# Kernel tuning notes

Measured on AMD Instinct MI355X. Metric: run time of the kernel, lower is better.

Reference implementation:

```python
import jax, jax.numpy as jnp
import numpy as np

Bsz, T, N, Dm = 4, 256, 32, 128
L, S, DC = 2, 16, 4          # num_layers, d_state, d_conv
DI = 2 * Dm                   # d_inner (expand=2)
DTR = Dm // 16                # dt_rank = ceil(128/16) = 8
K, R = 4, 16                  # K_bases, rank
MAX_DT = 0.2

def _silu(x):
    return x * jax.nn.sigmoid(x)

def _causal_dwconv(x, w, b):
    # x: [BN, T, DI], w: [DI, DC] depthwise, left-pad DC-1 (== pad DC-1 both sides then [:T])
    xc = jnp.swapaxes(x, 1, 2)  # [BN, DI, T]
    y = jax.lax.conv_general_dilated(xc, w[:, None, :], (1,), [(DC - 1, 0)],
                                     feature_group_count=DI,
                                     dimension_numbers=('NCH', 'OIH', 'NCH'))
    return jnp.swapaxes(y + b[None, :, None], 1, 2)

def _selective_scan(x, dt, Bm, Cm, A):
    # x, dt: [BN,T,DI]; Bm, Cm: [BN,T,S]; A: [DI,S]
    def step(carry, inp):
        dt_t, B_t, C_t, x_t = inp
        dA = jnp.exp(dt_t[:, :, None] * A)                      # [BN,DI,S]
        carry = dA * carry + dt_t[:, :, None] * B_t[:, None, :] * x_t[:, :, None]
        y = jnp.einsum('bds,bs->bd', carry, C_t)
        return carry, y
    BN = x.shape[0]
    carry0 = jnp.zeros((BN, DI, S), x.dtype)
    seq = (jnp.swapaxes(dt, 0, 1), jnp.swapaxes(Bm, 0, 1),
           jnp.swapaxes(Cm, 0, 1), jnp.swapaxes(x, 0, 1))
    _, ys = jax.lax.scan(step, carry0, seq)
    return jnp.swapaxes(ys, 0, 1)

def _mamba(h, in_w, cw, cb, xw, dtw, dtb, A_log, Dp, ow):
    xz = h @ in_w.T                          # [BN,T,2*DI]
    xh, z = xz[..., :DI], xz[..., DI:]
    xh = _silu(_causal_dwconv(xh, cw, cb))
    x_dbl = xh @ xw.T                        # [BN,T,DTR+2S]
    dt = jax.nn.softplus(x_dbl[..., :DTR] @ dtw.T + dtb)
    Bm = x_dbl[..., DTR:DTR + S]
    Cm = x_dbl[..., DTR + S:]
    A = -jnp.exp(A_log)
    y = _selective_scan(xh, dt, Bm, Cm, A) + Dp * xh
    return (y * _silu(z)) @ ow.T

def setup_inputs():
    ks = jax.random.split(jax.random.key(0), 32)
    n = lambda i, shp, s: jax.random.normal(ks[i], shp, jnp.float32) * s
    sD = 1.0 / np.sqrt(Dm); sI = 1.0 / np.sqrt(DI)
    return {
        'x': n(0, (Bsz, T, N, Dm), 1.0),
        'in_proj_w': n(1, (L, 2 * DI, Dm), sD),
        'conv_w': n(2, (L, DI, DC), 1.0 / np.sqrt(DC)),
        'conv_b': n(3, (L, DI), 0.01),
        'x_proj_w': n(4, (L, DTR + 2 * S, DI), sI),
        'dt_proj_w': n(5, (L, DI, DTR), 1.0 / np.sqrt(DTR)),
        'dt_proj_b': jnp.full((L, DI), -4.0, jnp.float32) + n(6, (L, DI), 0.1),
        'A_log': jnp.tile(jnp.log(jnp.arange(1, S + 1, dtype=jnp.float32))[None, None, :], (L, DI, 1)),
        'D_skip': jnp.ones((L, DI), jnp.float32),
        'out_proj_w': n(7, (L, Dm, DI), sI),
        'U': n(8, (K, Dm, R), sD),
        'V': n(9, (K, R, Dm), sD),
        'A_scale': jnp.full((K,), 0.3, jnp.float32),
        'gate_w1': n(10, (Dm, Dm), sD), 'gate_b1': jnp.zeros((Dm,), jnp.float32),
        'gate_w2': n(11, (K + 1, Dm), sD), 'gate_b2': jnp.zeros((K + 1,), jnp.float32),
        'film_g_w': n(12, (Dm, Dm), sD), 'film_g_b': jnp.zeros((Dm,), jnp.float32),
        'film_b_w': n(13, (Dm, Dm), sD), 'film_b_b': jnp.zeros((Dm,), jnp.float32),
        'mix_w1': n(14, (Dm, Dm), sD), 'mix_b1': jnp.zeros((Dm,), jnp.float32),
        'mix_w2': n(15, (1, Dm), sD), 'mix_b2': jnp.zeros((1,), jnp.float32),
    }

def reference(x, in_proj_w, conv_w, conv_b, x_proj_w, dt_proj_w, dt_proj_b, A_log, D_skip, out_proj_w, U, V, A_scale, gate_w1, gate_b1, gate_w2, gate_b2, film_g_w, film_g_b, film_b_w, film_b_b, mix_w1, mix_b1, mix_w2, mix_b2):
    B, T_, N_, D_ = x.shape
    h = x.transpose(0, 2, 1, 3).reshape(B * N_, T_, D_)   # [BN,T,D]
    for l in range(L):  # residual Mamba stack
        h = h + _mamba(h, in_proj_w[l], conv_w[l], conv_b[l], x_proj_w[l],
                       dt_proj_w[l], dt_proj_b[l], A_log[l], D_skip[l], out_proj_w[l])
    gate_out = jax.nn.gelu(h @ gate_w1.T + gate_b1, approximate=False) @ gate_w2.T + gate_b2
    w = jax.nn.softmax(gate_out[..., :K], axis=-1)        # [BN,T,K]
    dt = jax.nn.sigmoid(gate_out[..., K:]) * MAX_DT       # [BN,T,1]
    U_eff = U * A_scale[:, None, None]
    def amix(hh):
        hU = jnp.einsum('btd,kdr->btkr', hh, U_eff)
        hUV = jnp.einsum('btkr,krd->btkd', hU, V)
        return jnp.einsum('btkd,btk->btd', hUV, w)
    hA = amix(h)
    hA2 = amix(hA)  # taylor_order == 2
    upd_nl = jnp.tanh(dt * hA + 0.5 * dt ** 2 * hA2)
    gamma = jnp.tanh(h @ film_g_w.T + film_g_b)
    beta = jnp.tanh(h @ film_b_w.T + film_b_b)
    upd_nl = gamma * upd_nl + beta
    g = jax.nn.sigmoid(jax.nn.gelu(h @ mix_w1.T + mix_b1, approximate=False) @ mix_w2.T + mix_b2)
    h_dyn = h + g * upd_nl
    return h_dyn.reshape(B, N_, T_, D_).transpose(0, 2, 1, 3)
```

## Files before the change

kernel.cpp:

```cpp
#include <hip/hip_runtime.h>
#include <math.h>

#define BSZ   4
#define TT    256
#define NN    32
#define DM    128
#define LL    2
#define SS    16
#define DCV   4
#define DI    256
#define DTR   8
#define KK    4
#define RR    16
#define BN_   128
#define TOK   32768

typedef _Float16 f16x8 __attribute__((ext_vector_type(8)));
typedef float    f32x4 __attribute__((ext_vector_type(4)));

__device__ __forceinline__ float sigm(float x) { return __fdividef(1.f, 1.f + __expf(-x)); }

__global__ __launch_bounds__(256) void pack_h_k(const float* __restrict__ x, float* __restrict__ h)
{
    int tid = threadIdx.x;
    int d = tid & 127;
    int tok = blockIdx.x * 2 + (tid >> 7);
    int t = tok & 255;
    int bn = tok >> 8;
    int b = bn >> 5, n = bn & 31;
    h[(size_t)tok * DM + d] = x[(((size_t)b * TT + t) * NN + n) * DM + d];
}

template<int EPI, int ACT>
__global__ __launch_bounds__(256)
void mgemm_k(const float* __restrict__ A, int lda,
             const float* __restrict__ W,
             const float* __restrict__ bias,
             float* C, int ldc,
             int N, int K,
             const float* __restrict__ aux, int auxb)
{
    __shared__ char smem[24576];

    const int tid  = threadIdx.x;
    const int lane = tid & 63;
    const int wv   = tid >> 6;
    const long row0 = (long)blockIdx.y * 128;
    const int  colb = blockIdx.x * 64;
    const int  NC   = K >> 5;

    const int st_rc = tid >> 2;
    const int st_g  = tid & 3;
    const int offA0 = st_rc * 64        + ((st_g ^ (st_rc & 3)) << 4);
    const int offA1 = (st_rc + 64) * 64 + ((st_g ^ (st_rc & 3)) << 4);
    const int offW  = st_rc * 64        + ((st_g ^ (st_rc & 3)) << 4);
    const int wcol  = colb + st_rc;
    const bool wok  = (wcol < N);

    const int fr = lane & 15;
    const int fg = lane >> 4;
    const int ra0 = (wv << 5) + fr;
    const int offa0 = ra0 * 64        + ((fg ^ (ra0 & 3)) << 4);
    const int offa1 = (ra0 + 16) * 64 + ((fg ^ (ra0 & 3)) << 4);
    int offb[4];
#pragma unroll
    for (int nj = 0; nj < 4; ++nj) {
        int cb = (nj << 4) + fr;
        offb[nj] = cb * 64 + ((fg ^ (fr & 3)) << 4);
    }

    f32x4 acc[2][4];
#pragma unroll
    for (int mi = 0; mi < 2; ++mi)
#pragma unroll
        for (int nj = 0; nj < 4; ++nj) acc[mi][nj] = (f32x4){0.f, 0.f, 0.f, 0.f};

    float va0[8], va1[8], vw[8];

    {
        const float* pa0 = A + (row0 + st_rc) * (long)lda + st_g * 8;
        *(float4*)&va0[0] = *(const float4*)pa0;
        *(float4*)&va0[4] = *(const float4*)(pa0 + 4);
        const float* pa1 = pa0 + 64 * (long)lda;
        *(float4*)&va1[0] = *(const float4*)pa1;
        *(float4*)&va1[4] = *(const float4*)(pa1 + 4);
        if (wok) {
            const float* pw = W + (long)wcol * K + st_g * 8;
            *(float4*)&vw[0] = *(const float4*)pw;
            *(float4*)&vw[4] = *(const float4*)(pw + 4);
        } else {
#pragma unroll
            for (int j = 0; j < 8; ++j) vw[j] = 0.f;
        }
    }
    {
        char* base = smem;
        f16x8 h0, h1, hw;
#pragma unroll
        for (int j = 0; j < 8; ++j) { h0[j] = (_Float16)va0[j]; h1[j] = (_Float16)va1[j]; hw[j] = (_Float16)vw[j]; }
        *(f16x8*)(base + offA0) = h0;
        *(f16x8*)(base + offA1) = h1;
        *(f16x8*)(base + 8192 + offW) = hw;
    }
    __syncthreads();

    for (int c = 0; c < NC; ++c) {
        if (c + 1 < NC) {
            const int kk = (c + 1) << 5;
            const float* pa0 = A + (row0 + st_rc) * (long)lda + kk + st_g * 8;
            *(float4*)&va0[0] = *(const float4*)pa0;
            *(float4*)&va0[4] = *(const float4*)(pa0 + 4);
            const float* pa1 = pa0 + 64 * (long)lda;
            *(float4*)&va1[0] = *(const float4*)pa1;
            *(float4*)&va1[4] = *(const float4*)(pa1 + 4);
            if (wok) {
                const float* pw = W + (long)wcol * K + kk + st_g * 8;
                *(float4*)&vw[0] = *(const float4*)pw;
                *(float4*)&vw[4] = *(const float4*)(pw + 4);
            }
        }
        {
            const char* As = smem + (c & 1) * 12288;
            const char* Ws = As + 8192;
            f16x8 af0 = *(const f16x8*)(As + offa0);
            f16x8 af1 = *(const f16x8*)(As + offa1);
            f16x8 bf[4];
#pragma unroll
            for (int nj = 0; nj < 4; ++nj) bf[nj] = *(const f16x8*)(Ws + offb[nj]);
#pragma unroll
            for (int nj = 0; nj < 4; ++nj) {
                acc[0][nj] = __builtin_amdgcn_mfma_f32_16x16x32_f16(af0, bf[nj], acc[0][nj], 0, 0, 0);
                acc[1][nj] = __builtin_amdgcn_mfma_f32_16x16x32_f16(af1, bf[nj], acc[1][nj], 0, 0, 0);
            }
        }
        if (c + 1 < NC) {
            char* base = smem + ((c + 1) & 1) * 12288;
            f16x8 h0, h1, hw;
#pragma unroll
            for (int j = 0; j < 8; ++j) { h0[j] = (_Float16)va0[j]; h1[j] = (_Float16)va1[j]; hw[j] = (_Float16)vw[j]; }
            *(f16x8*)(base + offA0) = h0;
            *(f16x8*)(base + offA1) = h1;
            *(f16x8*)(base + 8192 + offW) = hw;
        }
        __syncthreads();
    }

#pragma unroll
    for (int nj = 0; nj < 4; ++nj) {
        int col = colb + (nj << 4) + fr;
        if (col < N) {
            float bb = 0.f;
            if (EPI == 1 && bias) bb = bias[col];
#pragma unroll
            for (int mi = 0; mi < 2; ++mi) {
                long rg = row0 + (wv << 5) + (mi << 4) + (fg << 2);
#pragma unroll
                for (int r = 0; r < 4; ++r) {
                    float v = acc[mi][nj][r];
                    if (EPI == 1) {
                        v += bb;
                        if (ACT == 1) v = 0.5f * v * (1.f + erff(v * 0.70710678118654752f));
                        else if (ACT == 2) v = tanhf(v);
                    } else if (EPI == 6) {
                        v *= aux[(rg + r) * 4 + ((col >> 4) + auxb)];
                    }
                    float* pc = C + (rg + r) * (long)ldc + col;
                    if (EPI == 4) *pc += v;
                    else          *pc = v;
                }
            }
        }
    }
}

template<int BM, int BN, int TM, int TN, int EPI>
__global__ __launch_bounds__(256)
void gemm_k(const float* __restrict__ A, int lda,
            const float* __restrict__ W,
            const float* __restrict__ bias,
            float* C, int ldc,
            int M, int N, int K,
            const float* __restrict__ aux)
{
    constexpr int BK = 16;
    constexpr int LDS_A = BM + 4;
    constexpr int LDS_B = BN + 4;
    static_assert((BM / TM) * (BN / TN) == 256, "256 threads");
    constexpr int NA = BM * BK / 1024;
    constexpr int NB = BN * BK / 1024;

    __shared__ float As[BK][LDS_A];
    __shared__ float Ws[BK][LDS_B];

    const int tid = threadIdx.x;
    constexpr int nx = BN / TN;
    const int tx = tid % nx, ty = tid / nx;
    const long row0 = (long)blockIdx.y * BM;
    const long col0 = (long)blockIdx.x * BN;

    float acc[TM][TN];
#pragma unroll
    for (int i = 0; i < TM; i++)
#pragma unroll
        for (int j = 0; j < TN; j++) acc[i][j] = 0.f;

    for (int kk = 0; kk < K; kk += BK) {
        float4 a_reg[NA], w_reg[NB];
#pragma unroll
        for (int i = 0; i < NA; ++i) {
            int idx = i * 1024 + tid * 4;
            int r = idx >> 4, k0 = idx & 15;
            int k = kk + k0;
            const float* p = A + (row0 + r) * (long)lda + k;
            a_reg[i] = *(const float4*)p;
        }
#pragma unroll
        for (int i = 0; i < NB; ++i) {
            int idx = i * 1024 + tid * 4;
            int r = idx >> 4, k0 = idx & 15;
            long gc = col0 + r;
            int k = kk + k0;
            if (gc < N) {
                const float* p = W + gc * (long)K + k;
                w_reg[i] = *(const float4*)p;
            } else w_reg[i] = make_float4(0.f, 0.f, 0.f, 0.f);
        }
        __syncthreads();
#pragma unroll
        for (int i = 0; i < NA; ++i) {
            int idx = i * 1024 + tid * 4;
            int r = idx >> 4, k0 = idx & 15;
            As[k0 + 0][r] = a_reg[i].x; As[k0 + 1][r] = a_reg[i].y;
            As[k0 + 2][r] = a_reg[i].z; As[k0 + 3][r] = a_reg[i].w;
        }
#pragma unroll
        for (int i = 0; i < NB; ++i) {
            int idx = i * 1024 + tid * 4;
            int r = idx >> 4, k0 = idx & 15;
            Ws[k0 + 0][r] = w_reg[i].x; Ws[k0 + 1][r] = w_reg[i].y;
            Ws[k0 + 2][r] = w_reg[i].z; Ws[k0 + 3][r] = w_reg[i].w;
        }
        __syncthreads();
#pragma unroll
        for (int k = 0; k < BK; ++k) {
            float a_f[TM], w_f[TN];
#pragma unroll
            for (int i = 0; i < TM; i += 4)
                *(float4*)&a_f[i] = *(const float4*)&As[k][ty * TM + i];
#pragma unroll
            for (int j = 0; j < TN; j += 4)
                *(float4*)&w_f[j] = *(const float4*)&Ws[k][tx * TN + j];
#pragma unroll
            for (int i = 0; i < TM; i++)
#pragma unroll
                for (int j = 0; j < TN; j++)
                    acc[i][j] = fmaf(a_f[i], w_f[j], acc[i][j]);
        }
    }
#pragma unroll
    for (int i = 0; i < TM; i++) {
        long r = row0 + ty * TM + i;
#pragma unroll
        for (int j = 0; j < TN; j++) {
            long c = col0 + tx * TN + j;
            if (c < N) C[r * ldc + c] = acc[i][j];
        }
    }
}

__global__ __launch_bounds__(256) void conv_silu_k(const float* __restrict__ xz,
                                                   const float* __restrict__ cw,
                                                   const float* __restrict__ cb,
                                                   float* __restrict__ xh)
{
    int c = threadIdx.x;
    int t0 = blockIdx.x << 2;
    int bn = blockIdx.y;
    float w0 = cw[c * 4 + 0], w1 = cw[c * 4 + 1], w2 = cw[c * 4 + 2], w3 = cw[c * 4 + 3];
    float bb = cb[c];
    size_t base = ((size_t)bn * TT + t0) * 512 + c;
    float xm3 = (t0 >= 3) ? xz[base - 1536] : 0.f;
    float xm2 = (t0 >= 2) ? xz[base - 1024] : 0.f;
    float xm1 = (t0 >= 1) ? xz[base - 512]  : 0.f;
    float x0 = xz[base];
    float x1 = xz[base + 512];
    float x2 = xz[base + 1024];
    float x3 = xz[base + 1536];
    float o0 = bb + w3 * x0 + w2 * xm1 + w1 * xm2 + w0 * xm3;
    float o1 = bb + w3 * x1 + w2 * x0  + w1 * xm1 + w0 * xm2;
    float o2 = bb + w3 * x2 + w2 * x1  + w1 * x0  + w0 * xm1;
    float o3 = bb + w3 * x3 + w2 * x2  + w1 * x1  + w0 * x0;
    size_t ob = ((size_t)bn * TT + t0) * DI + c;
    xh[ob]           = o0 * sigm(o0);
    xh[ob + DI]      = o1 * sigm(o1);
    xh[ob + 2 * DI]  = o2 * sigm(o2);
    xh[ob + 3 * DI]  = o3 * sigm(o3);
}

#define SCH 16
__global__ __launch_bounds__(512) void scan_k(const float* __restrict__ xz,
                                              const float* xhp,
                                              const float* __restrict__ xdbl,
                                              const float* __restrict__ dtw,
                                              const float* __restrict__ dtb,
                                              const float* __restrict__ A_log,
                                              const float* __restrict__ Dp,
                                              float* yg)
{
    __shared__ float sdt[2][SCH][128];
    __shared__ float sxv[2][SCH][128];
    __shared__ float szz[2][SCH][128];
    __shared__ float sbc[2][SCH][32];
    __shared__ float sxd[2][SCH][8];

    const int tid  = threadIdx.x;
    const int lane = tid & 63;
    const int wave = tid >> 6;
    const int sq   = lane >> 4;
    const int dloc = (wave << 4) + (lane & 15);
    const int bn   = blockIdx.y;
    const int dbase= blockIdx.x << 7;
    const int d    = dbase + dloc;
    const size_t tokb = (size_t)bn * TT;

    float A[4];
#pragma unroll
    for (int q = 0; q < 4; ++q)
        A[q] = -__expf(A_log[d * SS + sq * 4 + q]);
    const float Dv = Dp[d];

    float st[4];
#pragma unroll
    for (int q = 0; q < 4; ++q) st[q] = 0.f;

    const int st0 = tid >> 5;
    const int sc0 = (tid & 31) << 2;
    const int bstep = tid >> 3, bq = (tid & 7) << 2;
    const int xi = tid - 128;
    const int xr = xi >> 1, xc4 = (xi & 1) << 2;
    float4 rxv, rzz, rbc, rxd;

    const int dt_s  = tid >> 5;
    const int dt_d4 = (tid & 31) << 2;
    float dtwv[4][8];
    float dtbv[4];
#pragma unroll
    for (int j = 0; j < 4; ++j) {
        const float* p = dtw + (size_t)(dbase + dt_d4 + j) * 8;
        *(float4*)&dtwv[j][0] = *(const float4*)p;
        *(float4*)&dtwv[j][4] = *(const float4*)(p + 4);
        dtbv[j] = dtb[dbase + dt_d4 + j];
    }

#define STAGE_ISSUE(TB) do {                                              \
    size_t tb_ = tokb + (TB);                                             \
    rxv = *(const float4*)&xhp[(tb_ + st0) * DI + dbase + sc0];           \
    rzz = *(const float4*)&xz [(tb_ + st0) * 512 + 256 + dbase + sc0];    \
    if (tid < 128) rbc = *(const float4*)&xdbl[(tb_ + bstep) * 40 + 8 + bq]; \
    else if (tid < 160) rxd = *(const float4*)&xdbl[(tb_ + xr) * 40 + xc4]; \
} while (0)

#define STAGE_WRITE(B) do {                                               \
    *(float4*)&sxv[B][st0][sc0] = rxv;                                    \
    *(float4*)&szz[B][st0][sc0] = rzz;                                    \
    if (tid < 128) *(float4*)&sbc[B][bstep][bq] = rbc;                    \
    else if (tid < 160) *(float4*)&sxd[B][xr][xc4] = rxd;                 \
} while (0)

#define DT_COMPUTE(B) do {                                                \
    float4 o_;                                                            \
    _Pragma("unroll")                                                     \
    for (int j = 0; j < 4; ++j) {                                         \
        float v_ = dtbv[j];                                               \
        _Pragma("unroll")                                                 \
        for (int k = 0; k < 8; ++k)                                       \
            v_ = fmaf(sxd[B][dt_s][k], dtwv[j][k], v_);                   \
        o_[j] = fmaxf(v_, 0.f) + __logf(1.f + __expf(-fabsf(v_)));        \
    }                                                                     \
    *(float4*)&sdt[B][dt_s][dt_d4] = o_;                                  \
} while (0)

    STAGE_ISSUE(0);
    STAGE_WRITE(0);
    __syncthreads();
    DT_COMPUTE(0);
    __syncthreads();

    for (int c = 0; c < TT / SCH; ++c) {
        const int b = c & 1;
        const bool more = (c + 1 < TT / SCH);
        if (more) STAGE_ISSUE((c + 1) * SCH);
        const int tb = c * SCH;
#pragma unroll
        for (int s = 0; s < SCH; ++s) {
            float dt_c = sdt[b][s][dloc];
            float xv_c = sxv[b][s][dloc];
            float z_c  = szz[b][s][dloc];
            float4 B4 = *(const float4*)&sbc[b][s][sq << 2];
            float4 C4 = *(const float4*)&sbc[b][s][16 + (sq << 2)];

            float dtx = dt_c * xv_c;
            float dA0 = __expf(A[0] * dt_c);
            float dA1 = __expf(A[1] * dt_c);
            float dA2 = __expf(A[2] * dt_c);
            float dA3 = __expf(A[3] * dt_c);
            st[0] = fmaf(dA0, st[0], dtx * B4.x);
            st[1] = fmaf(dA1, st[1], dtx * B4.y);
            st[2] = fmaf(dA2, st[2], dtx * B4.z);
            st[3] = fmaf(dA3, st[3], dtx * B4.w);
            float y0 = st[0] * C4.x;
            float y1 = st[1] * C4.y;
            y0 = fmaf(st[2], C4.z, y0);
            y1 = fmaf(st[3], C4.w, y1);
            float y = y0 + y1;
            y += __shfl_xor(y, 16, 64);
            y += __shfl_xor(y, 32, 64);
            float zg = __fdividef(z_c, 1.f + __expf(-z_c));
            float outv = (y + Dv * xv_c) * zg;
            if (sq == 0) yg[(tokb + tb + s) * DI + d] = outv;
        }
        if (more) STAGE_WRITE(b ^ 1);
        __syncthreads();
        if (more) DT_COMPUTE(b ^ 1);
        __syncthreads();
    }
#undef STAGE_ISSUE
#undef STAGE_WRITE
#undef DT_COMPUTE
}

__global__ __launch_bounds__(256) void gate_k(const float* __restrict__ gmb,
                                              const float* __restrict__ gw2,
                                              const float* __restrict__ gb2,
                                              const float* __restrict__ mw2,
                                              const float* __restrict__ mb2,
                                              const float* __restrict__ Ascale,
                                              float* __restrict__ ws4,
                                              float* __restrict__ dts,
                                              float* __restrict__ gs)
{
    int l = threadIdx.x & 63;
    int tok = blockIdx.x * 4 + (threadIdx.x >> 6);
    const float* g1 = gmb + (size_t)tok * 512;
    float a0 = g1[l], a1 = g1[l + 64];
    float m0 = g1[128 + l], m1v = g1[192 + l];
    float p[5];
#pragma unroll
    for (int j = 0; j < 5; j++)
        p[j] = a0 * gw2[j * DM + l] + a1 * gw2[j * DM + l + 64];
    float q = m0 * mw2[l] + m1v * mw2[l + 64];
#pragma unroll
    for (int off = 32; off; off >>= 1) {
#pragma unroll
        for (int j = 0; j < 5; j++) p[j] += __shfl_xor(p[j], off, 64);
        q += __shfl_xor(q, off, 64);
    }
    if (l == 0) {
        float go[5];
#pragma unroll
        for (int j = 0; j < 5; j++) go[j] = p[j] + gb2[j];
        float mx = fmaxf(fmaxf(go[0], go[1]), fmaxf(go[2], go[3]));
        float e[4], sum = 0.f;
#pragma unroll
        for (int k = 0; k < 4; k++) { e[k] = expf(go[k] - mx); sum += e[k]; }
        float inv = 1.f / sum;
#pragma unroll
        for (int k = 0; k < 4; k++) ws4[(size_t)tok * 4 + k] = e[k] * inv * Ascale[k];
        dts[tok] = 0.2f * sigm(go[4]);
        gs[tok]  = sigm(q + mb2[0]);
    }
}

__global__ __launch_bounds__(256) void pack_uv_k(const float* __restrict__ U,
                                                 const float* __restrict__ V,
                                                 float* __restrict__ Wu,
                                                 float* __restrict__ Wv)
{
    int i = blockIdx.x * 256 + threadIdx.x;
    if (i < 8192) {
        int kr = i >> 7, d = i & 127;
        int k = kr >> 4, r = kr & 15;
        Wu[i] = U[((size_t)k * DM + d) * RR + r];
        int d2 = i >> 6, kr2 = i & 63;
        int k2 = kr2 >> 4, r2 = kr2 & 15;
        Wv[i] = V[((size_t)k2 * RR + r2) * DM + d2];
    }
}

__global__ __launch_bounds__(256) void pack_cat_k(const float* __restrict__ gw1,
                                                  const float* __restrict__ gb1,
                                                  const float* __restrict__ mw1,
                                                  const float* __restrict__ mb1,
                                                  const float* __restrict__ fgw,
                                                  const float* __restrict__ fgb,
                                                  const float* __restrict__ fbw,
                                                  const float* __restrict__ fbb,
                                                  float* __restrict__ Wcat,
                                                  float* __restrict__ bcat)
{
    int i = blockIdx.x * 256 + threadIdx.x;
    if (i < 65536) {
        int r = i >> 7, k = i & 127;
        int sel = r >> 7;
        int rr = r & 127;
        const float* src = (sel == 0) ? gw1 : (sel == 1) ? mw1 : (sel == 2) ? fgw : fbw;
        Wcat[i] = src[rr * DM + k];
    }
    if (i < 512) {
        int sel = i >> 7, rr = i & 127;
        const float* src = (sel == 0) ? gb1 : (sel == 1) ? mb1 : (sel == 2) ? fgb : fbb;
        bcat[i] = src[rr];
    }
}

__global__ __launch_bounds__(256) void combine_k(const float* __restrict__ h,
                                                 const float* __restrict__ hA,
                                                 const float* __restrict__ hA2,
                                                 const float* __restrict__ gmb,
                                                 const float* __restrict__ dts,
                                                 const float* __restrict__ gs,
                                                 float* __restrict__ out)
{
    int tid = threadIdx.x;
    int d = tid & 127;
    int tok = blockIdx.x * 2 + (tid >> 7);
    int t = tok & 255;
    int bn = tok >> 8;
    int b = bn >> 5, n = bn & 31;
    float dtv = dts[tok], gv = gs[tok];
    size_t i = (size_t)tok * DM + d;
    float u = tanhf(dtv * hA[i] + 0.5f * dtv * dtv * hA2[i]);
    float gamma = gmb[(size_t)tok * 512 + 256 + d];
    float beta  = gmb[(size_t)tok * 512 + 384 + d];
    u = gamma * u + beta;
    out[(((size_t)b * TT + t) * NN + n) * DM + d] = h[i] + gv * u;
}

extern "C" void kernel_launch(void* const* d_in, const int* in_sizes, int n_in,
                              void* d_out, int out_size, void* d_ws, size_t ws_size,
                              hipStream_t stream)
{
    const float* x       = (const float*)d_in[0];
    const float* in_w    = (const float*)d_in[1];
    const float* conv_w  = (const float*)d_in[2];
    const float* conv_b  = (const float*)d_in[3];
    const float* xpw     = (const float*)d_in[4];
    const float* dtw     = (const float*)d_in[5];
    const float* dtb     = (const float*)d_in[6];
    const float* A_log   = (const float*)d_in[7];
    const float* D_skip  = (const float*)d_in[8];
    const float* ow      = (const float*)d_in[9];
    const float* U       = (const float*)d_in[10];
    const float* V       = (const float*)d_in[11];
    const float* Ascale  = (const float*)d_in[12];
    const float* gw1     = (const float*)d_in[13];
    const float* gb1     = (const float*)d_in[14];
    const float* gw2     = (const float*)d_in[15];
    const float* gb2     = (const float*)d_in[16];
    const float* fgw     = (const float*)d_in[17];
    const float* fgb     = (const float*)d_in[18];
    const float* fbw     = (const float*)d_in[19];
    const float* fbb     = (const float*)d_in[20];
    const float* mw1     = (const float*)d_in[21];
    const float* mb1     = (const float*)d_in[22];
    const float* mw2     = (const float*)d_in[23];
    const float* mb2     = (const float*)d_in[24];

    float* ws = (float*)d_ws;
    float* h    = ws;
    float* xz   = h + 4194304;
    float* xh   = xz + 16777216;
    float* xdbl = xh + 8388608;

    pack_h_k<<<TOK / 2, 256, 0, stream>>>(x, h);

    for (int l = 0; l < LL; ++l) {
        const float* iw = in_w + (size_t)l * 512 * 128;
        mgemm_k<0,0><<<dim3(8,256), 256, 0, stream>>>(
            h, DM, iw, nullptr, xz, 512, 512, 128, nullptr, 0);
        conv_silu_k<<<dim3(TT / 4, BN_), 256, 0, stream>>>(
            xz, conv_w + (size_t)l * DI * DCV, conv_b + (size_t)l * DI, xh);
        gemm_k<64,64,4,4,0><<<dim3(1,512), 256, 0, stream>>>(
            xh, DI, xpw + (size_t)l * 40 * DI, nullptr, xdbl, 40, TOK, 40, DI, nullptr);
        scan_k<<<dim3(2, BN_), 512, 0, stream>>>(
            xz, xh, xdbl, dtw + (size_t)l * DI * DTR, dtb + (size_t)l * DI,
            A_log + (size_t)l * DI * SS, D_skip + (size_t)l * DI, xh);
        mgemm_k<4,0><<<dim3(2,256), 256, 0, stream>>>(
            xh, DI, ow + (size_t)l * DM * DI, nullptr, h, DM, 128, 256, nullptr, 0);
    }

    float* gmb  = xz;
    float* Zb   = xz;
    float* hA   = xh;
    float* hA2  = xh + 4194304;
    float* Wcat = xdbl;
    float* bcat = xdbl + 65536;
    float* Wu   = xdbl + 66048;
    float* Wv   = xdbl + 74240;
    float* ws4  = xdbl + 82432;
    float* dts  = xdbl + 213504;
    float* gs   = xdbl + 246272;

    pack_cat_k<<<256, 256, 0, stream>>>(gw1, gb1, mw1, mb1, fgw, fgb, fbw, fbb, Wcat, bcat);
    mgemm_k<1,1><<<dim3(4,256), 256, 0, stream>>>(
        h, DM, Wcat, bcat, gmb, 512, 256, 128, nullptr, 0);
    mgemm_k<1,2><<<dim3(4,256), 256, 0, stream>>>(
        h, DM, Wcat + 256 * 128, bcat + 256, gmb + 256, 512, 256, 128, nullptr, 0);
    gate_k<<<TOK / 4, 256, 0, stream>>>(gmb, gw2, gb2, mw2, mb2, Ascale, ws4, dts, gs);
    pack_uv_k<<<32, 256, 0, stream>>>(U, V, Wu, Wv);

    mgemm_k<6,0><<<dim3(1,256), 256, 0, stream>>>(
        h, DM, Wu, nullptr, Zb, 512, 64, 128, ws4, 0);
    mgemm_k<0,0><<<dim3(2,256), 256, 0, stream>>>(
        Zb, 512, Wv, nullptr, hA, DM, 128, 64, nullptr, 0);
    mgemm_k<6,0><<<dim3(1,256), 256, 0, stream>>>(
        hA, DM, Wu, nullptr, Zb, 512, 64, 128, ws4, 0);
    mgemm_k<0,0><<<dim3(2,256), 256, 0, stream>>>(
        Zb, 512, Wv, nullptr, hA2, DM, 128, 64, nullptr, 0);

    combine_k<<<TOK / 2, 256, 0, stream>>>(h, hA, hA2, gmb, dts, gs, (float*)d_out);
}
```

Before: 543.9 us.

## Fuse amix chain and combine into one MFMA kernel; split xz into halves

Replaces the four low-rank amix GEMM launches plus the combine kernel with a single kernel. It keeps a 128-token tile of h, the Wu/Wv weights and the intermediate Z and hA in LDS as fp16 and runs both Taylor-order passes with MFMA before applying the tanh/FiLM/gate epilogue. The in_proj GEMM now writes the x and z halves into separate contiguous buffers, so conv and scan read with a 256 stride instead of 512. SiLU on z moves into the scan's shared-memory staging step. The fused kernel uses 80KB of LDS, which limits occupancy, and hA is rounded to fp16 between the passes.

```diff
diff --git a/kernel.cpp b/kernel.cpp
--- a/kernel.cpp
+++ b/kernel.cpp
@@ -36,9 +36,8 @@
 void mgemm_k(const float* __restrict__ A, int lda,
              const float* __restrict__ W,
              const float* __restrict__ bias,
-             float* C, int ldc,
-             int N, int K,
-             const float* __restrict__ aux, int auxb)
+             float* C, float* C2, int ldc,
+             int N, int K)
 {
     __shared__ char smem[24576];
 
@@ -161,26 +160,28 @@
                         v += bb;
                         if (ACT == 1) v = 0.5f * v * (1.f + erff(v * 0.70710678118654752f));
                         else if (ACT == 2) v = tanhf(v);
-                    } else if (EPI == 6) {
-                        v *= aux[(rg + r) * 4 + ((col >> 4) + auxb)];
                     }
-                    float* pc = C + (rg + r) * (long)ldc + col;
-                    if (EPI == 4) *pc += v;
-                    else          *pc = v;
+                    if (EPI == 7) {
+                        float* pc = (col < 256) ? (C + (rg + r) * 256 + col)
+                                                : (C2 + (rg + r) * 256 + (col - 256));
+                        *pc = v;
+                    } else {
+                        float* pc = C + (rg + r) * (long)ldc + col;
+                        if (EPI == 4) *pc += v;
+                        else          *pc = v;
+                    }
                 }
             }
         }
     }
 }
 
-template<int BM, int BN, int TM, int TN, int EPI>
+template<int BM, int BN, int TM, int TN>
 __global__ __launch_bounds__(256)
 void gemm_k(const float* __restrict__ A, int lda,
             const float* __restrict__ W,
-            const float* __restrict__ bias,
             float* C, int ldc,
-            int M, int N, int K,
-            const float* __restrict__ aux)
+            int M, int N, int K)
 {
     constexpr int BK = 16;
     constexpr int LDS_A = BM + 4;
@@ -268,7 +269,7 @@
     }
 }
 
-__global__ __launch_bounds__(256) void conv_silu_k(const float* __restrict__ xz,
+__global__ __launch_bounds__(256) void conv_silu_k(const float* __restrict__ xhalf,
                                                    const float* __restrict__ cw,
                                                    const float* __restrict__ cb,
                                                    float* __restrict__ xh)
@@ -278,19 +279,19 @@
     int bn = blockIdx.y;
     float w0 = cw[c * 4 + 0], w1 = cw[c * 4 + 1], w2 = cw[c * 4 + 2], w3 = cw[c * 4 + 3];
     float bb = cb[c];
-    size_t base = ((size_t)bn * TT + t0) * 512 + c;
-    float xm3 = (t0 >= 3) ? xz[base - 1536] : 0.f;
-    float xm2 = (t0 >= 2) ? xz[base - 1024] : 0.f;
-    float xm1 = (t0 >= 1) ? xz[base - 512]  : 0.f;
-    float x0 = xz[base];
-    float x1 = xz[base + 512];
-    float x2 = xz[base + 1024];
-    float x3 = xz[base + 1536];
+    size_t base = ((size_t)bn * TT + t0) * DI + c;
+    float xm3 = (t0 >= 3) ? xhalf[base - 3 * DI] : 0.f;
+    float xm2 = (t0 >= 2) ? xhalf[base - 2 * DI] : 0.f;
+    float xm1 = (t0 >= 1) ? xhalf[base - DI]     : 0.f;
+    float x0 = xhalf[base];
+    float x1 = xhalf[base + DI];
+    float x2 = xhalf[base + 2 * DI];
+    float x3 = xhalf[base + 3 * DI];
     float o0 = bb + w3 * x0 + w2 * xm1 + w1 * xm2 + w0 * xm3;
     float o1 = bb + w3 * x1 + w2 * x0  + w1 * xm1 + w0 * xm2;
     float o2 = bb + w3 * x2 + w2 * x1  + w1 * x0  + w0 * xm1;
     float o3 = bb + w3 * x3 + w2 * x2  + w1 * x1  + w0 * x0;
-    size_t ob = ((size_t)bn * TT + t0) * DI + c;
+    size_t ob = base;
     xh[ob]           = o0 * sigm(o0);
     xh[ob + DI]      = o1 * sigm(o1);
     xh[ob + 2 * DI]  = o2 * sigm(o2);
@@ -298,7 +299,7 @@
 }
 
 #define SCH 16
-__global__ __launch_bounds__(512) void scan_k(const float* __restrict__ xz,
+__global__ __launch_bounds__(512) void scan_k(const float* __restrict__ zbuf,
                                               const float* xhp,
                                               const float* __restrict__ xdbl,
                                               const float* __restrict__ dtw,
@@ -354,15 +355,18 @@
 
 #define STAGE_ISSUE(TB) do {                                              \
     size_t tb_ = tokb + (TB);                                             \
-    rxv = *(const float4*)&xhp[(tb_ + st0) * DI + dbase + sc0];           \
-    rzz = *(const float4*)&xz [(tb_ + st0) * 512 + 256 + dbase + sc0];    \
+    rxv = *(const float4*)&xhp [(tb_ + st0) * DI + dbase + sc0];          \
+    rzz = *(const float4*)&zbuf[(tb_ + st0) * DI + dbase + sc0];          \
     if (tid < 128) rbc = *(const float4*)&xdbl[(tb_ + bstep) * 40 + 8 + bq]; \
     else if (tid < 160) rxd = *(const float4*)&xdbl[(tb_ + xr) * 40 + xc4]; \
 } while (0)
 
 #define STAGE_WRITE(B) do {                                               \
     *(float4*)&sxv[B][st0][sc0] = rxv;                                    \
-    *(float4*)&szz[B][st0][sc0] = rzz;                                    \
+    float4 zs_;                                                           \
+    zs_.x = rzz.x * sigm(rzz.x); zs_.y = rzz.y * sigm(rzz.y);             \
+    zs_.z = rzz.z * sigm(rzz.z); zs_.w = rzz.w * sigm(rzz.w);             \
+    *(float4*)&szz[B][st0][sc0] = zs_;                                    \
     if (tid < 128) *(float4*)&sbc[B][bstep][bq] = rbc;                    \
     else if (tid < 160) *(float4*)&sxd[B][xr][xc4] = rxd;                 \
 } while (0)
@@ -395,7 +399,7 @@
         for (int s = 0; s < SCH; ++s) {
             float dt_c = sdt[b][s][dloc];
             float xv_c = sxv[b][s][dloc];
-            float z_c  = szz[b][s][dloc];
+            float zg   = szz[b][s][dloc];
             float4 B4 = *(const float4*)&sbc[b][s][sq << 2];
             float4 C4 = *(const float4*)&sbc[b][s][16 + (sq << 2)];
 
@@ -415,7 +419,6 @@
             float y = y0 + y1;
             y += __shfl_xor(y, 16, 64);
             y += __shfl_xor(y, 32, 64);
-            float zg = __fdividef(z_c, 1.f + __expf(-z_c));
             float outv = (y + Dv * xv_c) * zg;
             if (sq == 0) yg[(tokb + tb + s) * DI + d] = outv;
         }
@@ -513,27 +516,203 @@
     }
 }
 
-__global__ __launch_bounds__(256) void combine_k(const float* __restrict__ h,
-                                                 const float* __restrict__ hA,
-                                                 const float* __restrict__ hA2,
-                                                 const float* __restrict__ gmb,
-                                                 const float* __restrict__ dts,
-                                                 const float* __restrict__ gs,
-                                                 float* __restrict__ out)
-{
-    int tid = threadIdx.x;
-    int d = tid & 127;
-    int tok = blockIdx.x * 2 + (tid >> 7);
-    int t = tok & 255;
-    int bn = tok >> 8;
-    int b = bn >> 5, n = bn & 31;
-    float dtv = dts[tok], gv = gs[tok];
-    size_t i = (size_t)tok * DM + d;
-    float u = tanhf(dtv * hA[i] + 0.5f * dtv * dtv * hA2[i]);
-    float gamma = gmb[(size_t)tok * 512 + 256 + d];
-    float beta  = gmb[(size_t)tok * 512 + 384 + d];
-    u = gamma * u + beta;
-    out[(((size_t)b * TT + t) * NN + n) * DM + d] = h[i] + gv * u;
+__global__ __launch_bounds__(256) void amix_combine_k(
+    const float* __restrict__ h,
+    const float* __restrict__ Wu,
+    const float* __restrict__ Wv,
+    const float* __restrict__ ws4,
+    const float* __restrict__ gmb,
+    const float* __restrict__ dts,
+    const float* __restrict__ gs,
+    float* __restrict__ out)
+{
+    __shared__ char smem[81920];
+    char* At  = smem;
+    char* Wus = smem + 32768;
+    char* Zt  = smem + 49152;
+    char* Wvs = smem + 65536;
+
+    const int tid  = threadIdx.x;
+    const int lane = tid & 63;
+    const int wv   = tid >> 6;
+    const long r0  = (long)blockIdx.x * 128;
+    const int fr = lane & 15;
+    const int fg = lane >> 4;
+
+#pragma unroll
+    for (int i = 0; i < 8; ++i) {
+        int idx = i * 256 + tid;
+        int row = idx >> 4, gk = idx & 15;
+        int c = gk >> 2, g = gk & 3;
+        const float* p = h + (r0 + row) * 128 + gk * 8;
+        float4 v0 = *(const float4*)p, v1 = *(const float4*)(p + 4);
+        f16x8 hv;
+        hv[0] = (_Float16)v0.x; hv[1] = (_Float16)v0.y; hv[2] = (_Float16)v0.z; hv[3] = (_Float16)v0.w;
+        hv[4] = (_Float16)v1.x; hv[5] = (_Float16)v1.y; hv[6] = (_Float16)v1.z; hv[7] = (_Float16)v1.w;
+        *(f16x8*)(At + c * 8192 + row * 64 + ((g ^ (row & 3)) << 4)) = hv;
+    }
+#pragma unroll
+    for (int i = 0; i < 4; ++i) {
+        int idx = i * 256 + tid;
+        int col = idx >> 4, gk = idx & 15;
+        int c = gk >> 2, g = gk & 3;
+        const float* p = Wu + col * 128 + gk * 8;
+        float4 v0 = *(const float4*)p, v1 = *(const float4*)(p + 4);
+        f16x8 hv;
+        hv[0] = (_Float16)v0.x; hv[1] = (_Float16)v0.y; hv[2] = (_Float16)v0.z; hv[3] = (_Float16)v0.w;
+        hv[4] = (_Float16)v1.x; hv[5] = (_Float16)v1.y; hv[6] = (_Float16)v1.z; hv[7] = (_Float16)v1.w;
+        *(f16x8*)(Wus + c * 4096 + col * 64 + ((g ^ (col & 3)) << 4)) = hv;
+    }
+#pragma unroll
+    for (int i = 0; i < 4; ++i) {
+        int idx = i * 256 + tid;
+        int col = idx >> 3, gk = idx & 7;
+        int c = gk >> 2, g = gk & 3;
+        const float* p = Wv + col * 64 + gk * 8;
+        float4 v0 = *(const float4*)p, v1 = *(const float4*)(p + 4);
+        f16x8 hv;
+        hv[0] = (_Float16)v0.x; hv[1] = (_Float16)v0.y; hv[2] = (_Float16)v0.z; hv[3] = (_Float16)v0.w;
+        hv[4] = (_Float16)v1.x; hv[5] = (_Float16)v1.y; hv[6] = (_Float16)v1.z; hv[7] = (_Float16)v1.w;
+        *(f16x8*)(Wvs + c * 8192 + col * 64 + ((g ^ (col & 3)) << 4)) = hv;
+    }
+    __syncthreads();
+
+    const int ra0 = (wv << 5) + fr;
+    const int ra1 = ra0 + 16;
+    const int offa0 = ra0 * 64 + ((fg ^ (ra0 & 3)) << 4);
+    const int offa1 = ra1 * 64 + ((fg ^ (ra1 & 3)) << 4);
+    int offbu[4];
+#pragma unroll
+    for (int nj = 0; nj < 4; ++nj) {
+        int cb = (nj << 4) + fr;
+        offbu[nj] = cb * 64 + ((fg ^ (fr & 3)) << 4);
+    }
+    int offbv[8];
+#pragma unroll
+    for (int nj = 0; nj < 8; ++nj) {
+        int cb = (nj << 4) + fr;
+        offbv[nj] = cb * 64 + ((fg ^ (fr & 3)) << 4);
+    }
+
+#define ZPASS(SRC, ACCZ) do {                                              \
+    _Pragma("unroll")                                                      \
+    for (int c = 0; c < 4; ++c) {                                          \
+        f16x8 a0 = *(const f16x8*)(SRC + c * 8192 + offa0);                \
+        f16x8 a1 = *(const f16x8*)(SRC + c * 8192 + offa1);                \
+        _Pragma("unroll")                                                  \
+        for (int nj = 0; nj < 4; ++nj) {                                   \
+            f16x8 bf = *(const f16x8*)(Wus + c * 4096 + offbu[nj]);        \
+            ACCZ[0][nj] = __builtin_amdgcn_mfma_f32_16x16x32_f16(a0, bf, ACCZ[0][nj], 0, 0, 0); \
+            ACCZ[1][nj] = __builtin_amdgcn_mfma_f32_16x16x32_f16(a1, bf, ACCZ[1][nj], 0, 0, 0); \
+        }                                                                  \
+    }                                                                      \
+} while (0)
+
+#define ZSCALE_STORE(ACCZ) do {                                            \
+    _Pragma("unroll")                                                      \
+    for (int mi = 0; mi < 2; ++mi) {                                       \
+        _Pragma("unroll")                                                  \
+        for (int r = 0; r < 4; ++r) {                                      \
+            int row = (wv << 5) + (mi << 4) + (fg << 2) + r;               \
+            const float* wp = ws4 + (r0 + row) * 4;                        \
+            _Pragma("unroll")                                              \
+            for (int nj = 0; nj < 4; ++nj) {                               \
+                float v = ACCZ[mi][nj][r] * wp[nj];                        \
+                int col = (nj << 4) + fr;                                  \
+                int c2 = col >> 5, g2 = (col >> 3) & 3, e2 = col & 7;      \
+                *(_Float16*)(Zt + c2 * 8192 + row * 64 +                   \
+                    ((g2 ^ (row & 3)) << 4) + e2 * 2) = (_Float16)v;       \
+            }                                                              \
+        }                                                                  \
+    }                                                                      \
+} while (0)
+
+#define VPASS(ACCV) do {                                                   \
+    _Pragma("unroll")                                                      \
+    for (int c = 0; c < 2; ++c) {                                          \
+        f16x8 a0 = *(const f16x8*)(Zt + c * 8192 + offa0);                 \
+        f16x8 a1 = *(const f16x8*)(Zt + c * 8192 + offa1);                 \
+        _Pragma("unroll")                                                  \
+        for (int nj = 0; nj < 8; ++nj) {                                   \
+            f16x8 bf = *(const f16x8*)(Wvs + c * 8192 + offbv[nj]);        \
+            ACCV[0][nj] = __builtin_amdgcn_mfma_f32_16x16x32_f16(a0, bf, ACCV[0][nj], 0, 0, 0); \
+            ACCV[1][nj] = __builtin_amdgcn_mfma_f32_16x16x32_f16(a1, bf, ACCV[1][nj], 0, 0, 0); \
+        }                                                                  \
+    }                                                                      \
+} while (0)
+
+    f32x4 accZ[2][4];
+#pragma unroll
+    for (int mi = 0; mi < 2; ++mi)
+#pragma unroll
+        for (int nj = 0; nj < 4; ++nj) accZ[mi][nj] = (f32x4){0.f, 0.f, 0.f, 0.f};
+    ZPASS(At, accZ);
+    ZSCALE_STORE(accZ);
+    __syncthreads();
+
+    f32x4 accA[2][8];
+#pragma unroll
+    for (int mi = 0; mi < 2; ++mi)
+#pragma unroll
+        for (int nj = 0; nj < 8; ++nj) accA[mi][nj] = (f32x4){0.f, 0.f, 0.f, 0.f};
+    VPASS(accA);
+#pragma unroll
+    for (int mi = 0; mi < 2; ++mi)
+#pragma unroll
+        for (int nj = 0; nj < 8; ++nj)
+#pragma unroll
+            for (int r = 0; r < 4; ++r) {
+                int row = (wv << 5) + (mi << 4) + (fg << 2) + r;
+                int col = (nj << 4) + fr;
+                int c3 = col >> 5, g3 = (col >> 3) & 3, e3 = col & 7;
+                *(_Float16*)(At + c3 * 8192 + row * 64 +
+                    ((g3 ^ (row & 3)) << 4) + e3 * 2) = (_Float16)accA[mi][nj][r];
+            }
+    __syncthreads();
+
+#pragma unroll
+    for (int mi = 0; mi < 2; ++mi)
+#pragma unroll
+        for (int nj = 0; nj < 4; ++nj) accZ[mi][nj] = (f32x4){0.f, 0.f, 0.f, 0.f};
+    ZPASS(At, accZ);
+    ZSCALE_STORE(accZ);
+    __syncthreads();
+
+    f32x4 accB[2][8];
+#pragma unroll
+    for (int mi = 0; mi < 2; ++mi)
+#pragma unroll
+        for (int nj = 0; nj < 8; ++nj) accB[mi][nj] = (f32x4){0.f, 0.f, 0.f, 0.f};
+    VPASS(accB);
+
+#pragma unroll
+    for (int mi = 0; mi < 2; ++mi) {
+#pragma unroll
+        for (int r = 0; r < 4; ++r) {
+            int row = (wv << 5) + (mi << 4) + (fg << 2) + r;
+            long tok = r0 + row;
+            float dtv = dts[tok], gv = gs[tok];
+            float hdt = 0.5f * dtv * dtv;
+            int t = (int)(tok & 255);
+            int bn = (int)(tok >> 8);
+            int b = bn >> 5, n = bn & 31;
+            float* orow = out + (((size_t)b * TT + t) * NN + n) * DM;
+            const float* hrow = h + tok * 128;
+            const float* grow = gmb + tok * 512;
+#pragma unroll
+            for (int nj = 0; nj < 8; ++nj) {
+                int col = (nj << 4) + fr;
+                float u = tanhf(dtv * accA[mi][nj][r] + hdt * accB[mi][nj][r]);
+                float gam = grow[256 + col];
+                float bet = grow[384 + col];
+                u = gam * u + bet;
+                orow[col] = hrow[col] + gv * u;
+            }
+        }
+    }
+#undef ZPASS
+#undef ZSCALE_STORE
+#undef VPASS
 }
 
 extern "C" void kernel_launch(void* const* d_in, const int* in_sizes, int n_in,
@@ -567,32 +746,31 @@
     const float* mb2     = (const float*)d_in[24];
 
     float* ws = (float*)d_ws;
-    float* h    = ws;
-    float* xz   = h + 4194304;
-    float* xh   = xz + 16777216;
-    float* xdbl = xh + 8388608;
+    float* h     = ws;
+    float* xz    = h + 4194304;
+    float* xhalf = xz;
+    float* zbuf  = xz + 8388608;
+    float* xh    = xz + 16777216;
+    float* xdbl  = xh + 8388608;
 
     pack_h_k<<<TOK / 2, 256, 0, stream>>>(x, h);
 
     for (int l = 0; l < LL; ++l) {
         const float* iw = in_w + (size_t)l * 512 * 128;
-        mgemm_k<0,0><<<dim3(8,256), 256, 0, stream>>>(
-            h, DM, iw, nullptr, xz, 512, 512, 128, nullptr, 0);
+        mgemm_k<7,0><<<dim3(8,256), 256, 0, stream>>>(
+            h, DM, iw, nullptr, xhalf, zbuf, 0, 512, 128);
         conv_silu_k<<<dim3(TT / 4, BN_), 256, 0, stream>>>(
-            xz, conv_w + (size_t)l * DI * DCV, conv_b + (size_t)l * DI, xh);
-        gemm_k<64,64,4,4,0><<<dim3(1,512), 256, 0, stream>>>(
-            xh, DI, xpw + (size_t)l * 40 * DI, nullptr, xdbl, 40, TOK, 40, DI, nullptr);
+            xhalf, conv_w + (size_t)l * DI * DCV, conv_b + (size_t)l * DI, xh);
+        gemm_k<64,64,4,4><<<dim3(1,512), 256, 0, stream>>>(
+            xh, DI, xpw + (size_t)l * 40 * DI, xdbl, 40, TOK, 40, DI);
         scan_k<<<dim3(2, BN_), 512, 0, stream>>>(
-            xz, xh, xdbl, dtw + (size_t)l * DI * DTR, dtb + (size_t)l * DI,
+            zbuf, xh, xdbl, dtw + (size_t)l * DI * DTR, dtb + (size_t)l * DI,
             A_log + (size_t)l * DI * SS, D_skip + (size_t)l * DI, xh);
         mgemm_k<4,0><<<dim3(2,256), 256, 0, stream>>>(
-            xh, DI, ow + (size_t)l * DM * DI, nullptr, h, DM, 128, 256, nullptr, 0);
+            xh, DI, ow + (size_t)l * DM * DI, nullptr, h, nullptr, DM, 128, 256);
     }
 
     float* gmb  = xz;
-    float* Zb   = xz;
-    float* hA   = xh;
-    float* hA2  = xh + 4194304;
     float* Wcat = xdbl;
     float* bcat = xdbl + 65536;
     float* Wu   = xdbl + 66048;
@@ -603,20 +781,12 @@
 
     pack_cat_k<<<256, 256, 0, stream>>>(gw1, gb1, mw1, mb1, fgw, fgb, fbw, fbb, Wcat, bcat);
     mgemm_k<1,1><<<dim3(4,256), 256, 0, stream>>>(
-        h, DM, Wcat, bcat, gmb, 512, 256, 128, nullptr, 0);
+        h, DM, Wcat, bcat, gmb, nullptr, 512, 256, 128);
     mgemm_k<1,2><<<dim3(4,256), 256, 0, stream>>>(
-        h, DM, Wcat + 256 * 128, bcat + 256, gmb + 256, 512, 256, 128, nullptr, 0);
+        h, DM, Wcat + 256 * 128, bcat + 256, gmb + 256, nullptr, 512, 256, 128);
     gate_k<<<TOK / 4, 256, 0, stream>>>(gmb, gw2, gb2, mw2, mb2, Ascale, ws4, dts, gs);
     pack_uv_k<<<32, 256, 0, stream>>>(U, V, Wu, Wv);
 
-    mgemm_k<6,0><<<dim3(1,256), 256, 0, stream>>>(
-        h, DM, Wu, nullptr, Zb, 512, 64, 128, ws4, 0);
-    mgemm_k<0,0><<<dim3(2,256), 256, 0, stream>>>(
-        Zb, 512, Wv, nullptr, hA, DM, 128, 64, nullptr, 0);
-    mgemm_k<6,0><<<dim3(1,256), 256, 0, stream>>>(
-        hA, DM, Wu, nullptr, Zb, 512, 64, 128, ws4, 0);
-    mgemm_k<0,0><<<dim3(2,256), 256, 0, stream>>>(
-        Zb, 512, Wv, nullptr, hA2, DM, 128, 64, nullptr, 0);
-
-    combine_k<<<TOK / 2, 256, 0, stream>>>(h, hA, hA2, gmb, dts, gs, (float*)d_out);
-}
+    amix_combine_k<<<TOK / 128, 256, 0, stream>>>(
+        h, Wu, Wv, ws4, gmb, dts, gs, (float*)d_out);
+}
```

Measured after the change: 505.8 us. 1.08x faster.
